# Kernel tuning notes

Measured on AMD Instinct MI355X. Metric: run time of the kernel, lower is better.

## Reference

```python
import jax, jax.numpy as jnp
import numpy as np

NEG_SLOPE = 0.2  # PyG GATConv LeakyReLU slope
BN_EPS = 1e-5
NUM_GRAPHS = 16


def gat_conv(x, src, dst, W, a_src, a_dst, bias, heads, out_c, concat):
    N = x.shape[0]
    h = (x @ W).reshape(N, heads, out_c)                      # [N,H,C]
    s_src = jnp.sum(h * a_src, axis=-1)                       # [N,H] per-node src score
    s_dst = jnp.sum(h * a_dst, axis=-1)                       # [N,H]
    e = jax.nn.leaky_relu(s_src[src] + s_dst[dst], NEG_SLOPE) # [E,H]
    # segment softmax over incoming edges of each dst node
    m = jax.ops.segment_max(e, dst, num_segments=N)           # [N,H]
    ex = jnp.exp(e - m[dst])
    denom = jax.ops.segment_sum(ex, dst, num_segments=N)      # [N,H]
    alpha = ex / (denom[dst] + 1e-16)                         # [E,H]
    msg = h[src] * alpha[:, :, None]                          # [E,H,C]
    out = jax.ops.segment_sum(msg, dst, num_segments=N)       # [N,H,C]
    out = out.reshape(N, heads * out_c) if concat else out.mean(axis=1)
    return out + bias


def batchnorm_eval(x, gamma, beta, rm, rv):
    return (x - rm) * jax.lax.rsqrt(rv + BN_EPS) * gamma + beta


def setup_inputs() -> dict:
    key = jax.random.key(0)
    ks = jax.random.split(key, 16)
    N, E, Fin, Hc, Hd, Emb = 20000, 640000, 128, 64, 4, 128
    x = jax.random.normal(ks[0], (N, Fin), dtype=jnp.float32)
    edge_index = jax.random.randint(ks[1], (2, E), 0, N, dtype=jnp.int64)
    batch = jnp.sort(jax.random.randint(ks[2], (N,), 0, NUM_GRAPHS, dtype=jnp.int64))
    sc1 = 1.0 / np.sqrt(Fin)
    sc2 = 1.0 / np.sqrt(Hc * Hd)
    return {
        "x": x, "edge_index": edge_index, "batch": batch,
        "W1": jax.random.normal(ks[3], (Fin, Hd * Hc), dtype=jnp.float32) * sc1,
        "a_src1": jax.random.normal(ks[4], (Hd, Hc), dtype=jnp.float32) * sc2,
        "a_dst1": jax.random.normal(ks[5], (Hd, Hc), dtype=jnp.float32) * sc2,
        "b1": jnp.zeros((Hd * Hc,), jnp.float32),
        "g1": jnp.ones((Hd * Hc,), jnp.float32),
        "be1": jnp.zeros((Hd * Hc,), jnp.float32),
        "rm1": jax.random.normal(ks[6], (Hd * Hc,), dtype=jnp.float32) * 0.1,
        "rv1": jnp.ones((Hd * Hc,), jnp.float32),
        "W2": jax.random.normal(ks[7], (Hd * Hc, Emb), dtype=jnp.float32) * sc2,
        "a_src2": jax.random.normal(ks[8], (1, Emb), dtype=jnp.float32) / np.sqrt(Emb),
        "a_dst2": jax.random.normal(ks[9], (1, Emb), dtype=jnp.float32) / np.sqrt(Emb),
        "b2": jnp.zeros((Emb,), jnp.float32),
        "g2": jnp.ones((Emb,), jnp.float32),
        "be2": jnp.zeros((Emb,), jnp.float32),
        "rm2": jax.random.normal(ks[10], (Emb,), dtype=jnp.float32) * 0.1,
        "rv2": jnp.ones((Emb,), jnp.float32),
    }


def reference(x, edge_index, batch, W1, a_src1, a_dst1, b1, g1, be1, rm1, rv1,
              W2, a_src2, a_dst2, b2, g2, be2, rm2, rv2):
    N = x.shape[0]
    loops = jnp.arange(N, dtype=edge_index.dtype)
    src = jnp.concatenate([edge_index[0], loops])  # PyG GATConv adds self-loops
    dst = jnp.concatenate([edge_index[1], loops])
    # layer 1: heads=4, concat
    h = gat_conv(x, src, dst, W1, a_src1, a_dst1, b1, heads=4, out_c=64, concat=True)
    h = batchnorm_eval(h, g1, be1, rm1, rv1)
    h = jax.nn.elu(h)  # dropout is identity in eval mode
    # layer 2: heads=1, no concat (mean over heads)
    h = gat_conv(h, src, dst, W2, a_src2, a_dst2, b2, heads=1, out_c=128, concat=False)
    h = batchnorm_eval(h, g2, be2, rm2, rv2)
    # global mean pool per graph
    sums = jax.ops.segment_sum(h, batch, num_segments=NUM_GRAPHS)
    cnts = jax.ops.segment_sum(jnp.ones((N,), h.dtype), batch, num_segments=NUM_GRAPHS)
    return sums / jnp.maximum(cnts, 1.0)[:, None]
```

## Files before the change

kernel.cpp:

```cpp
#include <hip/hip_runtime.h>
#include <hip/hip_bf16.h>
#include <math.h>

#define NEG_SLOPE 0.2f
#define BN_EPS 1e-5f
#define ELLW 128
#define SCLAMP 60.0f
#define LDP 68

typedef __attribute__((ext_vector_type(8))) short bf16x8;
typedef __attribute__((ext_vector_type(4))) float f32x4;

__device__ __forceinline__ void atomAddF(float* p, float v) { unsafeAtomicAdd(p, v); }
__device__ __forceinline__ float bf_lo(unsigned u) { return __uint_as_float(u << 16); }
__device__ __forceinline__ float bf_hi(unsigned u) { return __uint_as_float(u & 0xffff0000u); }
__device__ __forceinline__ float lk(float x) { return x > 0.f ? x : NEG_SLOPE * x; }
__device__ __forceinline__ float eexp(float x) { return __expf(fminf(x, SCLAMP)); }

__global__ __launch_bounds__(256) void prep_kernel(const float* __restrict__ x,
                                                   const float* __restrict__ W1,
                                                   const float* __restrict__ W2,
                                                   __hip_bfloat16* __restrict__ xbf,
                                                   __hip_bfloat16* __restrict__ WT1,
                                                   __hip_bfloat16* __restrict__ WT2,
                                                   int* __restrict__ zb, int zwords,
                                                   int n4) {
    int i = blockIdx.x * blockDim.x + threadIdx.x;
    if (i < n4) {
        float4 v = ((const float4*)x)[i];
        ushort4 st;
        st.x = __bfloat16_as_ushort(__float2bfloat16(v.x));
        st.y = __bfloat16_as_ushort(__float2bfloat16(v.y));
        st.z = __bfloat16_as_ushort(__float2bfloat16(v.z));
        st.w = __bfloat16_as_ushort(__float2bfloat16(v.w));
        *(ushort4*)(xbf + (size_t)i * 4) = st;
        return;
    }
    int j = i - n4;
    if (j < 128 * 256) {
        int k = j >> 8, n = j & 255;
        WT1[(size_t)n * 128 + k] = __float2bfloat16(W1[j]);
        return;
    }
    j -= 128 * 256;
    if (j < 256 * 128) {
        int k = j >> 7, n = j & 127;
        WT2[(size_t)n * 256 + k] = __float2bfloat16(W2[j]);
        return;
    }
    j -= 256 * 128;
    if (j < zwords) zb[j] = 0;
}

__global__ __launch_bounds__(256) void scatter_kernel(const int* __restrict__ src,
                                                      const int* __restrict__ dst,
                                                      int* __restrict__ cnt,
                                                      unsigned short* __restrict__ ell,
                                                      int N, int E, int Etot) {
    const int xcd = blockIdx.x & 7;
    const int slice = blockIdx.x >> 3;
    const int nslices = gridDim.x >> 3;
    const int d0 = (int)((long)xcd * N / 8);
    const int d1 = (int)((long)(xcd + 1) * N / 8);
    for (int e = slice * 256 + threadIdx.x; e < Etot; e += nslices * 256) {
        int d = (e < E) ? dst[e] : e - E;
        if (d < d0 || d >= d1) continue;
        int s = (e < E) ? src[e] : d;
        int pos = atomicAdd(cnt + d, 1);
        if (pos < ELLW) ell[(size_t)d * ELLW + pos] = (unsigned short)s;
    }
}

__global__ __launch_bounds__(256) void gemm_score_kernel(const __hip_bfloat16* __restrict__ A,
                                                         const __hip_bfloat16* __restrict__ BT,
                                                         __hip_bfloat16* __restrict__ C,
                                                         const float* __restrict__ asrc,
                                                         const float* __restrict__ adst,
                                                         float* __restrict__ ssrc,
                                                         float* __restrict__ sdst,
                                                         int M, int N, int K, int heads) {
    __shared__ __hip_bfloat16 As[64 * LDP];
    __shared__ __hip_bfloat16 Bs[64 * LDP];
    const int tid = threadIdx.x;
    const int w = tid >> 6;
    const int lane = tid & 63;
    const int q = lane >> 4;
    const int r16 = lane & 15;
    const int bm = blockIdx.y * 64;
    const int bn = blockIdx.x * 64;
    const int lrow = tid >> 3;
    const int lseg = tid & 7;
    f32x4 acc[4] = {};

    for (int k0 = 0; k0 < K; k0 += 64) {
#pragma unroll
        for (int half = 0; half < 2; ++half) {
            int row = lrow + half * 32;
            int ga = min(bm + row, M - 1);
            *(bf16x8*)(&As[row * LDP + lseg * 8]) =
                *(const bf16x8*)(A + (size_t)ga * K + k0 + lseg * 8);
            *(bf16x8*)(&Bs[row * LDP + lseg * 8]) =
                *(const bf16x8*)(BT + (size_t)(bn + row) * K + k0 + lseg * 8);
        }
        __syncthreads();
#pragma unroll
        for (int kk = 0; kk < 64; kk += 32) {
            bf16x8 a = *(const bf16x8*)(&As[(w * 16 + r16) * LDP + kk + q * 8]);
#pragma unroll
            for (int t = 0; t < 4; ++t) {
                bf16x8 b = *(const bf16x8*)(&Bs[(t * 16 + r16) * LDP + kk + q * 8]);
                acc[t] = __builtin_amdgcn_mfma_f32_16x16x32_bf16(a, b, acc[t], 0, 0, 0);
            }
        }
        __syncthreads();
    }
#pragma unroll
    for (int t = 0; t < 4; ++t)
#pragma unroll
        for (int r = 0; r < 4; ++r) {
            int row = bm + w * 16 + q * 4 + r;
            if (row < M)
                C[(size_t)row * N + bn + t * 16 + r16] = __float2bfloat16(acc[t][r]);
        }
    if (heads) {
        const int h = (heads == 4) ? blockIdx.x : 0;
        float asv[4], adv[4];
#pragma unroll
        for (int t = 0; t < 4; ++t) {
            int col = bn + t * 16 + r16;
            asv[t] = asrc[col]; adv[t] = adst[col];
        }
#pragma unroll
        for (int r = 0; r < 4; ++r) {
            int row = bm + w * 16 + q * 4 + r;
            float ss = 0.f, sd = 0.f;
#pragma unroll
            for (int t = 0; t < 4; ++t) { ss += acc[t][r] * asv[t]; sd += acc[t][r] * adv[t]; }
#pragma unroll
            for (int mask = 1; mask <= 8; mask <<= 1) {
                ss += __shfl_xor(ss, mask);
                sd += __shfl_xor(sd, mask);
            }
            if (r16 == 0 && row < M) {
                atomAddF(&ssrc[(size_t)row * heads + h], ss);
                atomAddF(&sdst[(size_t)row * heads + h], sd);
            }
        }
    }
}

__global__ __launch_bounds__(256) void fused1_kernel(const unsigned short* __restrict__ ell,
                                                     const int* __restrict__ cnt,
                                                     const float* __restrict__ ssrc,
                                                     const float* __restrict__ sdst,
                                                     const __hip_bfloat16* __restrict__ h1,
                                                     const float* __restrict__ b,
                                                     const float* __restrict__ g,
                                                     const float* __restrict__ be,
                                                     const float* __restrict__ rm,
                                                     const float* __restrict__ rv,
                                                     __hip_bfloat16* __restrict__ out1,
                                                     int N) {
    __shared__ float4 sex[4][ELLW];
    const int w = threadIdx.x >> 6;
    const int lane = threadIdx.x & 63;
    const int n = blockIdx.x * 4 + w;
    if (n >= N) return;
    const int degn = min(cnt[n], ELLW);
    const unsigned short* __restrict__ row = ell + (size_t)n * ELLW;
    const float4 sd4 = *(const float4*)(sdst + (size_t)n * 4);

    float4 d4 = {0.f, 0.f, 0.f, 0.f};
    for (int i = lane; i < degn; i += 64) {
        int s = row[i];
        float4 sc = *(const float4*)(ssrc + (size_t)s * 4);
        float4 e4;
        e4.x = eexp(lk(sc.x + sd4.x)); e4.y = eexp(lk(sc.y + sd4.y));
        e4.z = eexp(lk(sc.z + sd4.z)); e4.w = eexp(lk(sc.w + sd4.w));
        sex[w][i] = e4;
        d4.x += e4.x; d4.y += e4.y; d4.z += e4.z; d4.w += e4.w;
    }
#pragma unroll
    for (int o = 32; o; o >>= 1) {
        d4.x += __shfl_xor(d4.x, o); d4.y += __shfl_xor(d4.y, o);
        d4.z += __shfl_xor(d4.z, o); d4.w += __shfl_xor(d4.w, o);
    }

    const int h = lane >> 4, c16 = lane & 15;
    const int ch = h * 64 + c16 * 4;
    const float denh = h == 0 ? d4.x : h == 1 ? d4.y : h == 2 ? d4.z : d4.w;
    const float rden = 1.f / (denh + 1e-16f);
    const __hip_bfloat16* hbase = h1 + ch;
    const float* exw = (const float*)&sex[w][0];

    f32x4 acc = {0.f, 0.f, 0.f, 0.f};
    int i = 0;
    for (; i + 7 < degn; i += 8) {
        int s[8]; float a[8]; uint2 u[8];
#pragma unroll
        for (int k = 0; k < 8; ++k) { s[k] = row[i + k]; a[k] = exw[(i + k) * 4 + h]; }
#pragma unroll
        for (int k = 0; k < 8; ++k) u[k] = *(const uint2*)(hbase + (size_t)s[k] * 256);
#pragma unroll
        for (int k = 0; k < 8; ++k) {
            acc.x += a[k] * bf_lo(u[k].x); acc.y += a[k] * bf_hi(u[k].x);
            acc.z += a[k] * bf_lo(u[k].y); acc.w += a[k] * bf_hi(u[k].y);
        }
    }
    for (; i < degn; ++i) {
        int s0 = row[i];
        float a0 = exw[i * 4 + h];
        uint2 u0 = *(const uint2*)(hbase + (size_t)s0 * 256);
        acc.x += a0 * bf_lo(u0.x); acc.y += a0 * bf_hi(u0.x);
        acc.z += a0 * bf_lo(u0.y); acc.w += a0 * bf_hi(u0.y);
    }
    float4 bb = *(const float4*)(b + ch), gg = *(const float4*)(g + ch);
    float4 ee = *(const float4*)(be + ch), mm = *(const float4*)(rm + ch);
    float4 vv = *(const float4*)(rv + ch);
    float o0 = (acc.x * rden + bb.x - mm.x) * rsqrtf(vv.x + BN_EPS) * gg.x + ee.x;
    float o1 = (acc.y * rden + bb.y - mm.y) * rsqrtf(vv.y + BN_EPS) * gg.y + ee.y;
    float o2 = (acc.z * rden + bb.z - mm.z) * rsqrtf(vv.z + BN_EPS) * gg.z + ee.z;
    float o3 = (acc.w * rden + bb.w - mm.w) * rsqrtf(vv.w + BN_EPS) * gg.w + ee.w;
    o0 = o0 > 0.f ? o0 : expm1f(o0);
    o1 = o1 > 0.f ? o1 : expm1f(o1);
    o2 = o2 > 0.f ? o2 : expm1f(o2);
    o3 = o3 > 0.f ? o3 : expm1f(o3);
    ushort4 st;
    st.x = __bfloat16_as_ushort(__float2bfloat16(o0));
    st.y = __bfloat16_as_ushort(__float2bfloat16(o1));
    st.z = __bfloat16_as_ushort(__float2bfloat16(o2));
    st.w = __bfloat16_as_ushort(__float2bfloat16(o3));
    *(ushort4*)(out1 + (size_t)n * 256 + ch) = st;
}

__global__ __launch_bounds__(256) void fused2_kernel(const unsigned short* __restrict__ ell,
                                                     const int* __restrict__ cnt,
                                                     const float* __restrict__ ssrc,
                                                     const float* __restrict__ sdst,
                                                     const __hip_bfloat16* __restrict__ h2,
                                                     const float* __restrict__ b,
                                                     const float* __restrict__ g,
                                                     const float* __restrict__ be,
                                                     const float* __restrict__ rm,
                                                     const float* __restrict__ rv,
                                                     __hip_bfloat16* __restrict__ out2,
                                                     int N) {
    __shared__ float sex[4][ELLW];
    const int w = threadIdx.x >> 6;
    const int lane = threadIdx.x & 63;
    const int n = blockIdx.x * 4 + w;
    if (n >= N) return;
    const int degn = min(cnt[n], ELLW);
    const unsigned short* __restrict__ row = ell + (size_t)n * ELLW;
    const float sd = sdst[n];

    float den = 0.f;
    for (int i = lane; i < degn; i += 64) {
        int s = row[i];
        float e = eexp(lk(ssrc[s] + sd));
        sex[w][i] = e;
        den += e;
    }
#pragma unroll
    for (int o = 32; o; o >>= 1) den += __shfl_xor(den, o);
    const float rden = 1.f / (den + 1e-16f);

    const int ch = lane * 2;
    const __hip_bfloat16* hbase = h2 + ch;
    float ax = 0.f, ay = 0.f;
    int i = 0;
    for (; i + 7 < degn; i += 8) {
        int s[8]; float a[8]; unsigned u[8];
#pragma unroll
        for (int k = 0; k < 8; ++k) { s[k] = row[i + k]; a[k] = sex[w][i + k]; }
#pragma unroll
        for (int k = 0; k < 8; ++k) u[k] = *(const unsigned*)(hbase + (size_t)s[k] * 128);
#pragma unroll
        for (int k = 0; k < 8; ++k) { ax += a[k] * bf_lo(u[k]); ay += a[k] * bf_hi(u[k]); }
    }
    for (; i < degn; ++i) {
        int s0 = row[i];
        float a0 = sex[w][i];
        unsigned u0 = *(const unsigned*)(hbase + (size_t)s0 * 128);
        ax += a0 * bf_lo(u0); ay += a0 * bf_hi(u0);
    }
    float2 bb = *(const float2*)(b + ch), gg = *(const float2*)(g + ch);
    float2 ee = *(const float2*)(be + ch), mm = *(const float2*)(rm + ch);
    float2 vv = *(const float2*)(rv + ch);
    float ox = (ax * rden + bb.x - mm.x) * rsqrtf(vv.x + BN_EPS) * gg.x + ee.x;
    float oy = (ay * rden + bb.y - mm.y) * rsqrtf(vv.y + BN_EPS) * gg.y + ee.y;
    ushort2 st;
    st.x = __bfloat16_as_ushort(__float2bfloat16(ox));
    st.y = __bfloat16_as_ushort(__float2bfloat16(oy));
    *(ushort2*)(out2 + (size_t)n * 128 + ch) = st;
}

__global__ __launch_bounds__(128) void pool_kernel(const __hip_bfloat16* __restrict__ out2,
                                                   const int* __restrict__ batch,
                                                   float* __restrict__ pool,
                                                   int N, int npb) {
    const int j = threadIdx.x;
    int n0 = blockIdx.x * npb;
    int n1 = min(n0 + npb, N);
    if (n0 >= n1) return;
    int curg = batch[n0];
    float acc = 0.f;
    for (int n = n0; n < n1; ++n) {
        int gr = batch[n];
        if (gr != curg) {
            atomAddF(pool + (size_t)curg * 128 + j, acc);
            acc = 0.f; curg = gr;
        }
        acc += __bfloat162float(out2[(size_t)n * 128 + j]);
    }
    atomAddF(pool + (size_t)curg * 128 + j, acc);
}

__device__ __forceinline__ int lowerBound(const int* __restrict__ a, int n, int v) {
    int lo = 0, hi = n;
    while (lo < hi) {
        int mid = (lo + hi) >> 1;
        if (a[mid] < v) lo = mid + 1; else hi = mid;
    }
    return lo;
}

__global__ __launch_bounds__(256) void final_kernel(const float* __restrict__ pool,
                                                    const int* __restrict__ batch,
                                                    float* __restrict__ out, int N) {
    int i = blockIdx.x * blockDim.x + threadIdx.x;
    int g = i >> 7;
    int c = lowerBound(batch, N, g + 1) - lowerBound(batch, N, g);
    out[i] = pool[i] / fmaxf((float)c, 1.f);
}

extern "C" void kernel_launch(void* const* d_in, const int* in_sizes, int n_in,
                              void* d_out, int out_size, void* d_ws, size_t ws_size,
                              hipStream_t stream) {
    const float* x    = (const float*)d_in[0];
    const int* ei     = (const int*)d_in[1];
    const int* batch  = (const int*)d_in[2];
    const float* W1   = (const float*)d_in[3];
    const float* as1  = (const float*)d_in[4];
    const float* ad1  = (const float*)d_in[5];
    const float* b1   = (const float*)d_in[6];
    const float* g1   = (const float*)d_in[7];
    const float* be1  = (const float*)d_in[8];
    const float* rm1  = (const float*)d_in[9];
    const float* rv1  = (const float*)d_in[10];
    const float* W2   = (const float*)d_in[11];
    const float* as2  = (const float*)d_in[12];
    const float* ad2  = (const float*)d_in[13];
    const float* b2   = (const float*)d_in[14];
    const float* g2   = (const float*)d_in[15];
    const float* be2  = (const float*)d_in[16];
    const float* rm2  = (const float*)d_in[17];
    const float* rv2  = (const float*)d_in[18];
    float* out = (float*)d_out;

    const int N = in_sizes[0] / 128;
    const int E = in_sizes[1] / 2;
    const int Etot = E + N;
    const int* src = ei;
    const int* dst = ei + E;

    char* p = (char*)d_ws;
    auto alloc = [&](size_t bytes) { char* r = p; p += (bytes + 255) & ~(size_t)255; return r; };
    __hip_bfloat16* h1   = (__hip_bfloat16*)alloc((size_t)N * 256 * 2);
    __hip_bfloat16* out1 = (__hip_bfloat16*)alloc((size_t)N * 256 * 2);
    __hip_bfloat16* out2 = (__hip_bfloat16*)alloc((size_t)N * 128 * 2);
    __hip_bfloat16* xbf  = (__hip_bfloat16*)alloc((size_t)N * 128 * 2);
    __hip_bfloat16* WT1  = (__hip_bfloat16*)alloc(256 * 128 * 2);
    __hip_bfloat16* WT2  = (__hip_bfloat16*)alloc(128 * 256 * 2);
    const int zwords     = N * 10 + 2048 + N;
    char* zbase          = alloc((size_t)zwords * 4);
    float* ssrc1         = (float*)zbase;
    float* sdst1         = ssrc1 + (size_t)N * 4;
    float* ssrc2         = sdst1 + (size_t)N * 4;
    float* sdst2         = ssrc2 + N;
    float* pool          = sdst2 + N;
    int*   cnt           = (int*)(pool + 2048);
    unsigned short* ell  = (unsigned short*)alloc((size_t)N * ELLW * 2);
    __hip_bfloat16* h2   = h1;

    const int n4 = N * 128 / 4;
    const int ptot = n4 + 2 * 128 * 256 + zwords;
    prep_kernel<<<(ptot + 255) / 256, 256, 0, stream>>>(x, W1, W2, xbf, WT1, WT2,
                                                        (int*)zbase, zwords, n4);
    scatter_kernel<<<2048, 256, 0, stream>>>(src, dst, cnt, ell, N, E, Etot);

    gemm_score_kernel<<<dim3(256 / 64, (N + 63) / 64), 256, 0, stream>>>(
        xbf, WT1, h1, as1, ad1, ssrc1, sdst1, N, 256, 128, 4);
    fused1_kernel<<<(N + 3) / 4, 256, 0, stream>>>(ell, cnt, ssrc1, sdst1, h1,
                                                   b1, g1, be1, rm1, rv1, out1, N);
    gemm_score_kernel<<<dim3(128 / 64, (N + 63) / 64), 256, 0, stream>>>(
        out1, WT2, h2, as2, ad2, ssrc2, sdst2, N, 128, 256, 1);
    fused2_kernel<<<(N + 3) / 4, 256, 0, stream>>>(ell, cnt, ssrc2, sdst2, h2,
                                                   b2, g2, be2, rm2, rv2, out2, N);

    pool_kernel<<<(N + 19) / 20, 128, 0, stream>>>(out2, batch, pool, N, 20);
    final_kernel<<<8, 256, 0, stream>>>(pool, batch, out, N);
}
```

Baseline: 239.9 us.

## Widen neighbor gathers to 16B per lane and fuse pooling into layer-2 aggregation

```diff
diff --git a/kernel.cpp b/kernel.cpp
--- a/kernel.cpp
+++ b/kernel.cpp
@@ -16,6 +16,10 @@
 __device__ __forceinline__ float bf_hi(unsigned u) { return __uint_as_float(u & 0xffff0000u); }
 __device__ __forceinline__ float lk(float x) { return x > 0.f ? x : NEG_SLOPE * x; }
 __device__ __forceinline__ float eexp(float x) { return __expf(fminf(x, SCLAMP)); }
+__device__ __forceinline__ unsigned packbf(float lo, float hi) {
+    return (unsigned)__bfloat16_as_ushort(__float2bfloat16(lo)) |
+           ((unsigned)__bfloat16_as_ushort(__float2bfloat16(hi)) << 16);
+}
 
 __global__ __launch_bounds__(256) void prep_kernel(const float* __restrict__ x,
                                                    const float* __restrict__ W1,
@@ -161,7 +165,8 @@
                                                      const float* __restrict__ rv,
                                                      __hip_bfloat16* __restrict__ out1,
                                                      int N) {
-    __shared__ float4 sex[4][ELLW];
+    __shared__ float sex[4][ELLW * 4];
+    __shared__ unsigned soff[4][ELLW];
     const int w = threadIdx.x >> 6;
     const int lane = threadIdx.x & 63;
     const int n = blockIdx.x * 4 + w;
@@ -177,8 +182,14 @@
         float4 e4;
         e4.x = eexp(lk(sc.x + sd4.x)); e4.y = eexp(lk(sc.y + sd4.y));
         e4.z = eexp(lk(sc.z + sd4.z)); e4.w = eexp(lk(sc.w + sd4.w));
-        sex[w][i] = e4;
+        *(float4*)(&sex[w][i * 4]) = e4;
+        soff[w][i] = (unsigned)s << 9;
         d4.x += e4.x; d4.y += e4.y; d4.z += e4.z; d4.w += e4.w;
+    }
+    if (lane == 0 && (degn & 1)) {
+        float4 z = {0.f, 0.f, 0.f, 0.f};
+        *(float4*)(&sex[w][degn * 4]) = z;
+        soff[w][degn] = 0;
     }
 #pragma unroll
     for (int o = 32; o; o >>= 1) {
@@ -186,51 +197,74 @@
         d4.z += __shfl_xor(d4.z, o); d4.w += __shfl_xor(d4.w, o);
     }
 
-    const int h = lane >> 4, c16 = lane & 15;
-    const int ch = h * 64 + c16 * 4;
+    const int half = lane >> 5;
+    const int l32 = lane & 31;
+    const int ch = l32 * 8;
+    const int h = l32 >> 3;
+    const unsigned choff = (unsigned)(l32 * 16);
     const float denh = h == 0 ? d4.x : h == 1 ? d4.y : h == 2 ? d4.z : d4.w;
     const float rden = 1.f / (denh + 1e-16f);
-    const __hip_bfloat16* hbase = h1 + ch;
-    const float* exw = (const float*)&sex[w][0];
-
-    f32x4 acc = {0.f, 0.f, 0.f, 0.f};
+    const unsigned char* __restrict__ hb = (const unsigned char*)h1;
+    const int degp = (degn + 1) & ~1;
+
+    f32x4 a0 = {0.f, 0.f, 0.f, 0.f}, a1 = {0.f, 0.f, 0.f, 0.f};
     int i = 0;
-    for (; i + 7 < degn; i += 8) {
-        int s[8]; float a[8]; uint2 u[8];
-#pragma unroll
-        for (int k = 0; k < 8; ++k) { s[k] = row[i + k]; a[k] = exw[(i + k) * 4 + h]; }
-#pragma unroll
-        for (int k = 0; k < 8; ++k) u[k] = *(const uint2*)(hbase + (size_t)s[k] * 256);
-#pragma unroll
-        for (int k = 0; k < 8; ++k) {
-            acc.x += a[k] * bf_lo(u[k].x); acc.y += a[k] * bf_hi(u[k].x);
-            acc.z += a[k] * bf_lo(u[k].y); acc.w += a[k] * bf_hi(u[k].y);
-        }
-    }
-    for (; i < degn; ++i) {
-        int s0 = row[i];
-        float a0 = exw[i * 4 + h];
-        uint2 u0 = *(const uint2*)(hbase + (size_t)s0 * 256);
-        acc.x += a0 * bf_lo(u0.x); acc.y += a0 * bf_hi(u0.x);
-        acc.z += a0 * bf_lo(u0.y); acc.w += a0 * bf_hi(u0.y);
-    }
-    float4 bb = *(const float4*)(b + ch), gg = *(const float4*)(g + ch);
-    float4 ee = *(const float4*)(be + ch), mm = *(const float4*)(rm + ch);
-    float4 vv = *(const float4*)(rv + ch);
-    float o0 = (acc.x * rden + bb.x - mm.x) * rsqrtf(vv.x + BN_EPS) * gg.x + ee.x;
-    float o1 = (acc.y * rden + bb.y - mm.y) * rsqrtf(vv.y + BN_EPS) * gg.y + ee.y;
-    float o2 = (acc.z * rden + bb.z - mm.z) * rsqrtf(vv.z + BN_EPS) * gg.z + ee.z;
-    float o3 = (acc.w * rden + bb.w - mm.w) * rsqrtf(vv.w + BN_EPS) * gg.w + ee.w;
-    o0 = o0 > 0.f ? o0 : expm1f(o0);
-    o1 = o1 > 0.f ? o1 : expm1f(o1);
-    o2 = o2 > 0.f ? o2 : expm1f(o2);
-    o3 = o3 > 0.f ? o3 : expm1f(o3);
-    ushort4 st;
-    st.x = __bfloat16_as_ushort(__float2bfloat16(o0));
-    st.y = __bfloat16_as_ushort(__float2bfloat16(o1));
-    st.z = __bfloat16_as_ushort(__float2bfloat16(o2));
-    st.w = __bfloat16_as_ushort(__float2bfloat16(o3));
-    *(ushort4*)(out1 + (size_t)n * 256 + ch) = st;
+    for (; i + 8 <= degp; i += 8) {
+        unsigned off[4]; float av[4]; uint4 u[4];
+#pragma unroll
+        for (int k = 0; k < 4; ++k) {
+            int e = i + 2 * k + half;
+            off[k] = soff[w][e] + choff;
+            av[k] = sex[w][e * 4 + h];
+        }
+#pragma unroll
+        for (int k = 0; k < 4; ++k) u[k] = *(const uint4*)(hb + off[k]);
+#pragma unroll
+        for (int k = 0; k < 4; ++k) {
+            a0.x += av[k] * bf_lo(u[k].x); a0.y += av[k] * bf_hi(u[k].x);
+            a0.z += av[k] * bf_lo(u[k].y); a0.w += av[k] * bf_hi(u[k].y);
+            a1.x += av[k] * bf_lo(u[k].z); a1.y += av[k] * bf_hi(u[k].z);
+            a1.z += av[k] * bf_lo(u[k].w); a1.w += av[k] * bf_hi(u[k].w);
+        }
+    }
+    for (; i < degp; i += 2) {
+        int e = i + half;
+        unsigned off = soff[w][e] + choff;
+        float av = sex[w][e * 4 + h];
+        uint4 u = *(const uint4*)(hb + off);
+        a0.x += av * bf_lo(u.x); a0.y += av * bf_hi(u.x);
+        a0.z += av * bf_lo(u.y); a0.w += av * bf_hi(u.y);
+        a1.x += av * bf_lo(u.z); a1.y += av * bf_hi(u.z);
+        a1.z += av * bf_lo(u.w); a1.w += av * bf_hi(u.w);
+    }
+    a0.x += __shfl_xor(a0.x, 32); a0.y += __shfl_xor(a0.y, 32);
+    a0.z += __shfl_xor(a0.z, 32); a0.w += __shfl_xor(a0.w, 32);
+    a1.x += __shfl_xor(a1.x, 32); a1.y += __shfl_xor(a1.y, 32);
+    a1.z += __shfl_xor(a1.z, 32); a1.w += __shfl_xor(a1.w, 32);
+
+    float4 bb0 = *(const float4*)(b + ch),  bb1 = *(const float4*)(b + ch + 4);
+    float4 gg0 = *(const float4*)(g + ch),  gg1 = *(const float4*)(g + ch + 4);
+    float4 ee0 = *(const float4*)(be + ch), ee1 = *(const float4*)(be + ch + 4);
+    float4 mm0 = *(const float4*)(rm + ch), mm1 = *(const float4*)(rm + ch + 4);
+    float4 vv0 = *(const float4*)(rv + ch), vv1 = *(const float4*)(rv + ch + 4);
+    float o0 = (a0.x * rden + bb0.x - mm0.x) * rsqrtf(vv0.x + BN_EPS) * gg0.x + ee0.x;
+    float o1 = (a0.y * rden + bb0.y - mm0.y) * rsqrtf(vv0.y + BN_EPS) * gg0.y + ee0.y;
+    float o2 = (a0.z * rden + bb0.z - mm0.z) * rsqrtf(vv0.z + BN_EPS) * gg0.z + ee0.z;
+    float o3 = (a0.w * rden + bb0.w - mm0.w) * rsqrtf(vv0.w + BN_EPS) * gg0.w + ee0.w;
+    float o4 = (a1.x * rden + bb1.x - mm1.x) * rsqrtf(vv1.x + BN_EPS) * gg1.x + ee1.x;
+    float o5 = (a1.y * rden + bb1.y - mm1.y) * rsqrtf(vv1.y + BN_EPS) * gg1.y + ee1.y;
+    float o6 = (a1.z * rden + bb1.z - mm1.z) * rsqrtf(vv1.z + BN_EPS) * gg1.z + ee1.z;
+    float o7 = (a1.w * rden + bb1.w - mm1.w) * rsqrtf(vv1.w + BN_EPS) * gg1.w + ee1.w;
+    o0 = o0 > 0.f ? o0 : expm1f(o0); o1 = o1 > 0.f ? o1 : expm1f(o1);
+    o2 = o2 > 0.f ? o2 : expm1f(o2); o3 = o3 > 0.f ? o3 : expm1f(o3);
+    o4 = o4 > 0.f ? o4 : expm1f(o4); o5 = o5 > 0.f ? o5 : expm1f(o5);
+    o6 = o6 > 0.f ? o6 : expm1f(o6); o7 = o7 > 0.f ? o7 : expm1f(o7);
+    if (half == 0) {
+        uint4 st;
+        st.x = packbf(o0, o1); st.y = packbf(o2, o3);
+        st.z = packbf(o4, o5); st.w = packbf(o6, o7);
+        *(uint4*)(out1 + (size_t)n * 256 + ch) = st;
+    }
 }
 
 __global__ __launch_bounds__(256) void fused2_kernel(const unsigned short* __restrict__ ell,
@@ -243,9 +277,11 @@
                                                      const float* __restrict__ be,
                                                      const float* __restrict__ rm,
                                                      const float* __restrict__ rv,
-                                                     __hip_bfloat16* __restrict__ out2,
+                                                     const int* __restrict__ batch,
+                                                     float* __restrict__ pool,
                                                      int N) {
     __shared__ float sex[4][ELLW];
+    __shared__ unsigned soff[4][ELLW];
     const int w = threadIdx.x >> 6;
     const int lane = threadIdx.x & 63;
     const int n = blockIdx.x * 4 + w;
@@ -259,61 +295,62 @@
         int s = row[i];
         float e = eexp(lk(ssrc[s] + sd));
         sex[w][i] = e;
+        soff[w][i] = (unsigned)s << 8;
         den += e;
     }
+    if (lane == 0 && (degn & 1)) { sex[w][degn] = 0.f; soff[w][degn] = 0; }
 #pragma unroll
     for (int o = 32; o; o >>= 1) den += __shfl_xor(den, o);
     const float rden = 1.f / (den + 1e-16f);
 
-    const int ch = lane * 2;
-    const __hip_bfloat16* hbase = h2 + ch;
-    float ax = 0.f, ay = 0.f;
+    const int half = lane >> 5;
+    const int l32 = lane & 31;
+    const int ch = l32 * 4;
+    const unsigned choff = (unsigned)(l32 * 8);
+    const unsigned char* __restrict__ hb = (const unsigned char*)h2;
+    const int degp = (degn + 1) & ~1;
+
+    f32x4 acc = {0.f, 0.f, 0.f, 0.f};
     int i = 0;
-    for (; i + 7 < degn; i += 8) {
-        int s[8]; float a[8]; unsigned u[8];
-#pragma unroll
-        for (int k = 0; k < 8; ++k) { s[k] = row[i + k]; a[k] = sex[w][i + k]; }
-#pragma unroll
-        for (int k = 0; k < 8; ++k) u[k] = *(const unsigned*)(hbase + (size_t)s[k] * 128);
-#pragma unroll
-        for (int k = 0; k < 8; ++k) { ax += a[k] * bf_lo(u[k]); ay += a[k] * bf_hi(u[k]); }
-    }
-    for (; i < degn; ++i) {
-        int s0 = row[i];
-        float a0 = sex[w][i];
-        unsigned u0 = *(const unsigned*)(hbase + (size_t)s0 * 128);
-        ax += a0 * bf_lo(u0); ay += a0 * bf_hi(u0);
-    }
-    float2 bb = *(const float2*)(b + ch), gg = *(const float2*)(g + ch);
-    float2 ee = *(const float2*)(be + ch), mm = *(const float2*)(rm + ch);
-    float2 vv = *(const float2*)(rv + ch);
-    float ox = (ax * rden + bb.x - mm.x) * rsqrtf(vv.x + BN_EPS) * gg.x + ee.x;
-    float oy = (ay * rden + bb.y - mm.y) * rsqrtf(vv.y + BN_EPS) * gg.y + ee.y;
-    ushort2 st;
-    st.x = __bfloat16_as_ushort(__float2bfloat16(ox));
-    st.y = __bfloat16_as_ushort(__float2bfloat16(oy));
-    *(ushort2*)(out2 + (size_t)n * 128 + ch) = st;
-}
-
-__global__ __launch_bounds__(128) void pool_kernel(const __hip_bfloat16* __restrict__ out2,
-                                                   const int* __restrict__ batch,
-                                                   float* __restrict__ pool,
-                                                   int N, int npb) {
-    const int j = threadIdx.x;
-    int n0 = blockIdx.x * npb;
-    int n1 = min(n0 + npb, N);
-    if (n0 >= n1) return;
-    int curg = batch[n0];
-    float acc = 0.f;
-    for (int n = n0; n < n1; ++n) {
-        int gr = batch[n];
-        if (gr != curg) {
-            atomAddF(pool + (size_t)curg * 128 + j, acc);
-            acc = 0.f; curg = gr;
-        }
-        acc += __bfloat162float(out2[(size_t)n * 128 + j]);
-    }
-    atomAddF(pool + (size_t)curg * 128 + j, acc);
+    for (; i + 8 <= degp; i += 8) {
+        unsigned off[4]; float av[4]; uint2 u[4];
+#pragma unroll
+        for (int k = 0; k < 4; ++k) {
+            int e = i + 2 * k + half;
+            off[k] = soff[w][e] + choff;
+            av[k] = sex[w][e];
+        }
+#pragma unroll
+        for (int k = 0; k < 4; ++k) u[k] = *(const uint2*)(hb + off[k]);
+#pragma unroll
+        for (int k = 0; k < 4; ++k) {
+            acc.x += av[k] * bf_lo(u[k].x); acc.y += av[k] * bf_hi(u[k].x);
+            acc.z += av[k] * bf_lo(u[k].y); acc.w += av[k] * bf_hi(u[k].y);
+        }
+    }
+    for (; i < degp; i += 2) {
+        int e = i + half;
+        unsigned off = soff[w][e] + choff;
+        float av = sex[w][e];
+        uint2 u = *(const uint2*)(hb + off);
+        acc.x += av * bf_lo(u.x); acc.y += av * bf_hi(u.x);
+        acc.z += av * bf_lo(u.y); acc.w += av * bf_hi(u.y);
+    }
+    acc.x += __shfl_xor(acc.x, 32); acc.y += __shfl_xor(acc.y, 32);
+    acc.z += __shfl_xor(acc.z, 32); acc.w += __shfl_xor(acc.w, 32);
+
+    if (half == 0) {
+        float4 bb = *(const float4*)(b + ch), gg = *(const float4*)(g + ch);
+        float4 ee = *(const float4*)(be + ch), mm = *(const float4*)(rm + ch);
+        float4 vv = *(const float4*)(rv + ch);
+        float o0 = (acc.x * rden + bb.x - mm.x) * rsqrtf(vv.x + BN_EPS) * gg.x + ee.x;
+        float o1 = (acc.y * rden + bb.y - mm.y) * rsqrtf(vv.y + BN_EPS) * gg.y + ee.y;
+        float o2 = (acc.z * rden + bb.z - mm.z) * rsqrtf(vv.z + BN_EPS) * gg.z + ee.z;
+        float o3 = (acc.w * rden + bb.w - mm.w) * rsqrtf(vv.w + BN_EPS) * gg.w + ee.w;
+        float* pp = pool + (size_t)batch[n] * 128 + ch;
+        atomAddF(pp + 0, o0); atomAddF(pp + 1, o1);
+        atomAddF(pp + 2, o2); atomAddF(pp + 3, o3);
+    }
 }
 
 __device__ __forceinline__ int lowerBound(const int* __restrict__ a, int n, int v) {
@@ -368,7 +405,6 @@
     auto alloc = [&](size_t bytes) { char* r = p; p += (bytes + 255) & ~(size_t)255; return r; };
     __hip_bfloat16* h1   = (__hip_bfloat16*)alloc((size_t)N * 256 * 2);
     __hip_bfloat16* out1 = (__hip_bfloat16*)alloc((size_t)N * 256 * 2);
-    __hip_bfloat16* out2 = (__hip_bfloat16*)alloc((size_t)N * 128 * 2);
     __hip_bfloat16* xbf  = (__hip_bfloat16*)alloc((size_t)N * 128 * 2);
     __hip_bfloat16* WT1  = (__hip_bfloat16*)alloc(256 * 128 * 2);
     __hip_bfloat16* WT2  = (__hip_bfloat16*)alloc(128 * 256 * 2);
@@ -396,8 +432,7 @@
     gemm_score_kernel<<<dim3(128 / 64, (N + 63) / 64), 256, 0, stream>>>(
         out1, WT2, h2, as2, ad2, ssrc2, sdst2, N, 128, 256, 1);
     fused2_kernel<<<(N + 3) / 4, 256, 0, stream>>>(ell, cnt, ssrc2, sdst2, h2,
-                                                   b2, g2, be2, rm2, rv2, out2, N);
-
-    pool_kernel<<<(N + 19) / 20, 128, 0, stream>>>(out2, batch, pool, N, 20);
+                                                   b2, g2, be2, rm2, rv2, batch, pool, N);
+
     final_kernel<<<8, 256, 0, stream>>>(pool, batch, out, N);
 }
```

After: 462.9 us. +93.0%, slower.

## Store GEMM output head-sliced, split aggregation per head, merge scatter with GEMM

Applied to the files above, without the earlier changes.

```diff
diff --git a/kernel.cpp b/kernel.cpp
--- a/kernel.cpp
+++ b/kernel.cpp
@@ -16,6 +16,10 @@
 __device__ __forceinline__ float bf_hi(unsigned u) { return __uint_as_float(u & 0xffff0000u); }
 __device__ __forceinline__ float lk(float x) { return x > 0.f ? x : NEG_SLOPE * x; }
 __device__ __forceinline__ float eexp(float x) { return __expf(fminf(x, SCLAMP)); }
+__device__ __forceinline__ unsigned packbf(float lo, float hi) {
+    return (unsigned)__bfloat16_as_ushort(__float2bfloat16(lo)) |
+           ((unsigned)__bfloat16_as_ushort(__float2bfloat16(hi)) << 16);
+}
 
 __global__ __launch_bounds__(256) void prep_kernel(const float* __restrict__ x,
                                                    const float* __restrict__ W1,
@@ -52,14 +56,108 @@
     if (j < zwords) zb[j] = 0;
 }
 
-__global__ __launch_bounds__(256) void scatter_kernel(const int* __restrict__ src,
-                                                      const int* __restrict__ dst,
-                                                      int* __restrict__ cnt,
-                                                      unsigned short* __restrict__ ell,
-                                                      int N, int E, int Etot) {
-    const int xcd = blockIdx.x & 7;
-    const int slice = blockIdx.x >> 3;
-    const int nslices = gridDim.x >> 3;
+__device__ __forceinline__ void gemm_body(const __hip_bfloat16* __restrict__ A,
+                                          const __hip_bfloat16* __restrict__ BT,
+                                          __hip_bfloat16* __restrict__ C,
+                                          const float* __restrict__ asrc,
+                                          const float* __restrict__ adst,
+                                          float* __restrict__ ssrc,
+                                          float* __restrict__ sdst,
+                                          int M, int N, int K, int heads,
+                                          int bx, int by) {
+    __shared__ __hip_bfloat16 As[64 * LDP];
+    __shared__ __hip_bfloat16 Bs[64 * LDP];
+    const int tid = threadIdx.x;
+    const int w = tid >> 6;
+    const int lane = tid & 63;
+    const int q = lane >> 4;
+    const int r16 = lane & 15;
+    const int bm = by * 64;
+    const int bn = bx * 64;
+    const int lrow = tid >> 3;
+    const int lseg = tid & 7;
+    f32x4 acc[4] = {};
+
+    for (int k0 = 0; k0 < K; k0 += 64) {
+#pragma unroll
+        for (int half = 0; half < 2; ++half) {
+            int row = lrow + half * 32;
+            int ga = min(bm + row, M - 1);
+            *(bf16x8*)(&As[row * LDP + lseg * 8]) =
+                *(const bf16x8*)(A + (size_t)ga * K + k0 + lseg * 8);
+            *(bf16x8*)(&Bs[row * LDP + lseg * 8]) =
+                *(const bf16x8*)(BT + (size_t)(bn + row) * K + k0 + lseg * 8);
+        }
+        __syncthreads();
+#pragma unroll
+        for (int kk = 0; kk < 64; kk += 32) {
+            bf16x8 a = *(const bf16x8*)(&As[(w * 16 + r16) * LDP + kk + q * 8]);
+#pragma unroll
+            for (int t = 0; t < 4; ++t) {
+                bf16x8 b = *(const bf16x8*)(&Bs[(t * 16 + r16) * LDP + kk + q * 8]);
+                acc[t] = __builtin_amdgcn_mfma_f32_16x16x32_bf16(a, b, acc[t], 0, 0, 0);
+            }
+        }
+        __syncthreads();
+    }
+    const size_t sbase = (size_t)(bn >> 6) * M * 64;
+#pragma unroll
+    for (int t = 0; t < 4; ++t)
+#pragma unroll
+        for (int r = 0; r < 4; ++r) {
+            int row = bm + w * 16 + q * 4 + r;
+            if (row < M)
+                C[sbase + (size_t)row * 64 + t * 16 + r16] = __float2bfloat16(acc[t][r]);
+        }
+    if (heads) {
+        const int h = (heads == 4) ? bx : 0;
+        float asv[4], adv[4];
+#pragma unroll
+        for (int t = 0; t < 4; ++t) {
+            int col = bn + t * 16 + r16;
+            asv[t] = asrc[col]; adv[t] = adst[col];
+        }
+#pragma unroll
+        for (int r = 0; r < 4; ++r) {
+            int row = bm + w * 16 + q * 4 + r;
+            float ss = 0.f, sd = 0.f;
+#pragma unroll
+            for (int t = 0; t < 4; ++t) { ss += acc[t][r] * asv[t]; sd += acc[t][r] * adv[t]; }
+#pragma unroll
+            for (int mask = 1; mask <= 8; mask <<= 1) {
+                ss += __shfl_xor(ss, mask);
+                sd += __shfl_xor(sd, mask);
+            }
+            if (r16 == 0 && row < M) {
+                atomAddF(&ssrc[(size_t)row * heads + h], ss);
+                atomAddF(&sdst[(size_t)row * heads + h], sd);
+            }
+        }
+    }
+}
+
+__global__ __launch_bounds__(256) void sg1_kernel(const __hip_bfloat16* __restrict__ A,
+                                                  const __hip_bfloat16* __restrict__ BT,
+                                                  __hip_bfloat16* __restrict__ C,
+                                                  const float* __restrict__ asrc,
+                                                  const float* __restrict__ adst,
+                                                  float* __restrict__ ssrc,
+                                                  float* __restrict__ sdst,
+                                                  int M, int nbg,
+                                                  const int* __restrict__ src,
+                                                  const int* __restrict__ dst,
+                                                  int* __restrict__ cnt,
+                                                  unsigned short* __restrict__ ell,
+                                                  int N, int E, int Etot) {
+    const int gb = blockIdx.x;
+    if (gb < nbg) {
+        gemm_body(A, BT, C, asrc, adst, ssrc, sdst, M, 256, 128, 4, gb & 3, gb >> 2);
+        return;
+    }
+    const int xcd = gb & 7;
+    const int sb = gb - nbg;
+    const int slice = sb >> 3;
+    const int nslices = (gridDim.x - nbg) >> 3;
     const int d0 = (int)((long)xcd * N / 8);
     const int d1 = (int)((long)(xcd + 1) * N / 8);
     for (int e = slice * 256 + threadIdx.x; e < Etot; e += nslices * 256) {
@@ -79,74 +177,7 @@
                                                          float* __restrict__ ssrc,
                                                          float* __restrict__ sdst,
                                                          int M, int N, int K, int heads) {
-    __shared__ __hip_bfloat16 As[64 * LDP];
-    __shared__ __hip_bfloat16 Bs[64 * LDP];
-    const int tid = threadIdx.x;
-    const int w = tid >> 6;
-    const int lane = tid & 63;
-    const int q = lane >> 4;
-    const int r16 = lane & 15;
-    const int bm = blockIdx.y * 64;
-    const int bn = blockIdx.x * 64;
-    const int lrow = tid >> 3;
-    const int lseg = tid & 7;
-    f32x4 acc[4] = {};
-
-    for (int k0 = 0; k0 < K; k0 += 64) {
-#pragma unroll
-        for (int half = 0; half < 2; ++half) {
-            int row = lrow + half * 32;
-            int ga = min(bm + row, M - 1);
-            *(bf16x8*)(&As[row * LDP + lseg * 8]) =
-                *(const bf16x8*)(A + (size_t)ga * K + k0 + lseg * 8);
-            *(bf16x8*)(&Bs[row * LDP + lseg * 8]) =
-                *(const bf16x8*)(BT + (size_t)(bn + row) * K + k0 + lseg * 8);
-        }
-        __syncthreads();
-#pragma unroll
-        for (int kk = 0; kk < 64; kk += 32) {
-            bf16x8 a = *(const bf16x8*)(&As[(w * 16 + r16) * LDP + kk + q * 8]);
-#pragma unroll
-            for (int t = 0; t < 4; ++t) {
-                bf16x8 b = *(const bf16x8*)(&Bs[(t * 16 + r16) * LDP + kk + q * 8]);
-                acc[t] = __builtin_amdgcn_mfma_f32_16x16x32_bf16(a, b, acc[t], 0, 0, 0);
-            }
-        }
-        __syncthreads();
-    }
-#pragma unroll
-    for (int t = 0; t < 4; ++t)
-#pragma unroll
-        for (int r = 0; r < 4; ++r) {
-            int row = bm + w * 16 + q * 4 + r;
-            if (row < M)
-                C[(size_t)row * N + bn + t * 16 + r16] = __float2bfloat16(acc[t][r]);
-        }
-    if (heads) {
-        const int h = (heads == 4) ? blockIdx.x : 0;
-        float asv[4], adv[4];
-#pragma unroll
-        for (int t = 0; t < 4; ++t) {
-            int col = bn + t * 16 + r16;
-            asv[t] = asrc[col]; adv[t] = adst[col];
-        }
-#pragma unroll
-        for (int r = 0; r < 4; ++r) {
-            int row = bm + w * 16 + q * 4 + r;
-            float ss = 0.f, sd = 0.f;
-#pragma unroll
-            for (int t = 0; t < 4; ++t) { ss += acc[t][r] * asv[t]; sd += acc[t][r] * adv[t]; }
-#pragma unroll
-            for (int mask = 1; mask <= 8; mask <<= 1) {
-                ss += __shfl_xor(ss, mask);
-                sd += __shfl_xor(sd, mask);
-            }
-            if (r16 == 0 && row < M) {
-                atomAddF(&ssrc[(size_t)row * heads + h], ss);
-                atomAddF(&sdst[(size_t)row * heads + h], sd);
-            }
-        }
-    }
+    gemm_body(A, BT, C, asrc, adst, ssrc, sdst, M, N, K, heads, blockIdx.x, blockIdx.y);
 }
 
 __global__ __launch_bounds__(256) void fused1_kernel(const unsigned short* __restrict__ ell,
@@ -161,76 +192,82 @@
                                                      const float* __restrict__ rv,
                                                      __hip_bfloat16* __restrict__ out1,
                                                      int N) {
-    __shared__ float4 sex[4][ELLW];
+    __shared__ float sex[4][ELLW];
+    __shared__ unsigned soff[4][ELLW];
     const int w = threadIdx.x >> 6;
     const int lane = threadIdx.x & 63;
     const int n = blockIdx.x * 4 + w;
+    const int h = blockIdx.y;
     if (n >= N) return;
     const int degn = min(cnt[n], ELLW);
     const unsigned short* __restrict__ row = ell + (size_t)n * ELLW;
-    const float4 sd4 = *(const float4*)(sdst + (size_t)n * 4);
-
-    float4 d4 = {0.f, 0.f, 0.f, 0.f};
+    const float sd = sdst[n * 4 + h];
+
+    float den = 0.f;
     for (int i = lane; i < degn; i += 64) {
         int s = row[i];
-        float4 sc = *(const float4*)(ssrc + (size_t)s * 4);
-        float4 e4;
-        e4.x = eexp(lk(sc.x + sd4.x)); e4.y = eexp(lk(sc.y + sd4.y));
-        e4.z = eexp(lk(sc.z + sd4.z)); e4.w = eexp(lk(sc.w + sd4.w));
-        sex[w][i] = e4;
-        d4.x += e4.x; d4.y += e4.y; d4.z += e4.z; d4.w += e4.w;
-    }
-#pragma unroll
-    for (int o = 32; o; o >>= 1) {
-        d4.x += __shfl_xor(d4.x, o); d4.y += __shfl_xor(d4.y, o);
-        d4.z += __shfl_xor(d4.z, o); d4.w += __shfl_xor(d4.w, o);
-    }
-
-    const int h = lane >> 4, c16 = lane & 15;
-    const int ch = h * 64 + c16 * 4;
-    const float denh = h == 0 ? d4.x : h == 1 ? d4.y : h == 2 ? d4.z : d4.w;
-    const float rden = 1.f / (denh + 1e-16f);
-    const __hip_bfloat16* hbase = h1 + ch;
-    const float* exw = (const float*)&sex[w][0];
-
-    f32x4 acc = {0.f, 0.f, 0.f, 0.f};
-    int i = 0;
-    for (; i + 7 < degn; i += 8) {
-        int s[8]; float a[8]; uint2 u[8];
-#pragma unroll
-        for (int k = 0; k < 8; ++k) { s[k] = row[i + k]; a[k] = exw[(i + k) * 4 + h]; }
-#pragma unroll
-        for (int k = 0; k < 8; ++k) u[k] = *(const uint2*)(hbase + (size_t)s[k] * 256);
-#pragma unroll
-        for (int k = 0; k < 8; ++k) {
-            acc.x += a[k] * bf_lo(u[k].x); acc.y += a[k] * bf_hi(u[k].x);
-            acc.z += a[k] * bf_lo(u[k].y); acc.w += a[k] * bf_hi(u[k].y);
-        }
-    }
-    for (; i < degn; ++i) {
-        int s0 = row[i];
-        float a0 = exw[i * 4 + h];
-        uint2 u0 = *(const uint2*)(hbase + (size_t)s0 * 256);
-        acc.x += a0 * bf_lo(u0.x); acc.y += a0 * bf_hi(u0.x);
-        acc.z += a0 * bf_lo(u0.y); acc.w += a0 * bf_hi(u0.y);
-    }
-    float4 bb = *(const float4*)(b + ch), gg = *(const float4*)(g + ch);
-    float4 ee = *(const float4*)(be + ch), mm = *(const float4*)(rm + ch);
-    float4 vv = *(const float4*)(rv + ch);
-    float o0 = (acc.x * rden + bb.x - mm.x) * rsqrtf(vv.x + BN_EPS) * gg.x + ee.x;
-    float o1 = (acc.y * rden + bb.y - mm.y) * rsqrtf(vv.y + BN_EPS) * gg.y + ee.y;
-    float o2 = (acc.z * rden + bb.z - mm.z) * rsqrtf(vv.z + BN_EPS) * gg.z + ee.z;
-    float o3 = (acc.w * rden + bb.w - mm.w) * rsqrtf(vv.w + BN_EPS) * gg.w + ee.w;
-    o0 = o0 > 0.f ? o0 : expm1f(o0);
-    o1 = o1 > 0.f ? o1 : expm1f(o1);
-    o2 = o2 > 0.f ? o2 : expm1f(o2);
-    o3 = o3 > 0.f ? o3 : expm1f(o3);
-    ushort4 st;
-    st.x = __bfloat16_as_ushort(__float2bfloat16(o0));
-    st.y = __bfloat16_as_ushort(__float2bfloat16(o1));
-    st.z = __bfloat16_as_ushort(__float2bfloat16(o2));
-    st.w = __bfloat16_as_ushort(__float2bfloat16(o3));
-    *(ushort4*)(out1 + (size_t)n * 256 + ch) = st;
+        float e = eexp(lk(ssrc[s * 4 + h] + sd));
+        sex[w][i] = e;
+        soff[w][i] = (unsigned)s << 7;
+        den += e;
+    }
+    const int degp = (degn + 15) & ~15;
+    for (int i = degn + lane; i < degp; i += 64) { sex[w][i] = 0.f; soff[w][i] = 0; }
+#pragma unroll
+    for (int o = 32; o; o >>= 1) den += __shfl_xor(den, o);
+    const float rden = 1.f / (den + 1e-16f);
+
+    const int eg = lane >> 3;
+    const int cc = lane & 7;
+    const unsigned choff = (unsigned)cc * 16;
+    const unsigned char* __restrict__ hb =
+        (const unsigned char*)(h1 + (size_t)h * N * 64);
+
+    float acc[8] = {};
+    for (int i = 0; i < degp; i += 16) {
+        int e0 = i + eg, e1 = i + 8 + eg;
+        float av0 = sex[w][e0], av1 = sex[w][e1];
+        unsigned o0 = soff[w][e0] + choff, o1 = soff[w][e1] + choff;
+        uint4 u0 = *(const uint4*)(hb + o0);
+        uint4 u1 = *(const uint4*)(hb + o1);
+        acc[0] += av0 * bf_lo(u0.x); acc[1] += av0 * bf_hi(u0.x);
+        acc[2] += av0 * bf_lo(u0.y); acc[3] += av0 * bf_hi(u0.y);
+        acc[4] += av0 * bf_lo(u0.z); acc[5] += av0 * bf_hi(u0.z);
+        acc[6] += av0 * bf_lo(u0.w); acc[7] += av0 * bf_hi(u0.w);
+        acc[0] += av1 * bf_lo(u1.x); acc[1] += av1 * bf_hi(u1.x);
+        acc[2] += av1 * bf_lo(u1.y); acc[3] += av1 * bf_hi(u1.y);
+        acc[4] += av1 * bf_lo(u1.z); acc[5] += av1 * bf_hi(u1.z);
+        acc[6] += av1 * bf_lo(u1.w); acc[7] += av1 * bf_hi(u1.w);
+    }
+#pragma unroll
+    for (int m = 8; m <= 32; m <<= 1)
+#pragma unroll
+        for (int j = 0; j < 8; ++j) acc[j] += __shfl_xor(acc[j], m);
+
+    if (eg == 0) {
+        const int ch = h * 64 + cc * 8;
+        float4 bb0 = *(const float4*)(b + ch),  bb1 = *(const float4*)(b + ch + 4);
+        float4 gg0 = *(const float4*)(g + ch),  gg1 = *(const float4*)(g + ch + 4);
+        float4 ee0 = *(const float4*)(be + ch), ee1 = *(const float4*)(be + ch + 4);
+        float4 mm0 = *(const float4*)(rm + ch), mm1 = *(const float4*)(rm + ch + 4);
+        float4 vv0 = *(const float4*)(rv + ch), vv1 = *(const float4*)(rv + ch + 4);
+        float o0 = (acc[0] * rden + bb0.x - mm0.x) * rsqrtf(vv0.x + BN_EPS) * gg0.x + ee0.x;
+        float o1 = (acc[1] * rden + bb0.y - mm0.y) * rsqrtf(vv0.y + BN_EPS) * gg0.y + ee0.y;
+        float o2 = (acc[2] * rden + bb0.z - mm0.z) * rsqrtf(vv0.z + BN_EPS) * gg0.z + ee0.z;
+        float o3 = (acc[3] * rden + bb0.w - mm0.w) * rsqrtf(vv0.w + BN_EPS) * gg0.w + ee0.w;
+        float o4 = (acc[4] * rden + bb1.x - mm1.x) * rsqrtf(vv1.x + BN_EPS) * gg1.x + ee1.x;
+        float o5 = (acc[5] * rden + bb1.y - mm1.y) * rsqrtf(vv1.y + BN_EPS) * gg1.y + ee1.y;
+        float o6 = (acc[6] * rden + bb1.z - mm1.z) * rsqrtf(vv1.z + BN_EPS) * gg1.z + ee1.z;
+        float o7 = (acc[7] * rden + bb1.w - mm1.w) * rsqrtf(vv1.w + BN_EPS) * gg1.w + ee1.w;
+        o0 = o0 > 0.f ? o0 : expm1f(o0); o1 = o1 > 0.f ? o1 : expm1f(o1);
+        o2 = o2 > 0.f ? o2 : expm1f(o2); o3 = o3 > 0.f ? o3 : expm1f(o3);
+        o4 = o4 > 0.f ? o4 : expm1f(o4); o5 = o5 > 0.f ? o5 : expm1f(o5);
+        o6 = o6 > 0.f ? o6 : expm1f(o6); o7 = o7 > 0.f ? o7 : expm1f(o7);
+        uint4 st;
+        st.x = packbf(o0, o1); st.y = packbf(o2, o3);
+        st.z = packbf(o4, o5); st.w = packbf(o6, o7);
+        *(uint4*)(out1 + (size_t)n * 256 + ch) = st;
+    }
 }
 
 __global__ __launch_bounds__(256) void fused2_kernel(const unsigned short* __restrict__ ell,
@@ -246,9 +283,11 @@
                                                      __hip_bfloat16* __restrict__ out2,
                                                      int N) {
     __shared__ float sex[4][ELLW];
+    __shared__ unsigned soff[4][ELLW];
     const int w = threadIdx.x >> 6;
     const int lane = threadIdx.x & 63;
     const int n = blockIdx.x * 4 + w;
+    const int hf = blockIdx.y;
     if (n >= N) return;
     const int degn = min(cnt[n], ELLW);
     const unsigned short* __restrict__ row = ell + (size_t)n * ELLW;
@@ -259,40 +298,62 @@
         int s = row[i];
         float e = eexp(lk(ssrc[s] + sd));
         sex[w][i] = e;
+        soff[w][i] = (unsigned)s << 7;
         den += e;
     }
+    const int degp = (degn + 15) & ~15;
+    for (int i = degn + lane; i < degp; i += 64) { sex[w][i] = 0.f; soff[w][i] = 0; }
 #pragma unroll
     for (int o = 32; o; o >>= 1) den += __shfl_xor(den, o);
     const float rden = 1.f / (den + 1e-16f);
 
-    const int ch = lane * 2;
-    const __hip_bfloat16* hbase = h2 + ch;
-    float ax = 0.f, ay = 0.f;
-    int i = 0;
-    for (; i + 7 < degn; i += 8) {
-        int s[8]; float a[8]; unsigned u[8];
-#pragma unroll
-        for (int k = 0; k < 8; ++k) { s[k] = row[i + k]; a[k] = sex[w][i + k]; }
-#pragma unroll
-        for (int k = 0; k < 8; ++k) u[k] = *(const unsigned*)(hbase + (size_t)s[k] * 128);
-#pragma unroll
-        for (int k = 0; k < 8; ++k) { ax += a[k] * bf_lo(u[k]); ay += a[k] * bf_hi(u[k]); }
-    }
-    for (; i < degn; ++i) {
-        int s0 = row[i];
-        float a0 = sex[w][i];
-        unsigned u0 = *(const unsigned*)(hbase + (size_t)s0 * 128);
-        ax += a0 * bf_lo(u0); ay += a0 * bf_hi(u0);
-    }
-    float2 bb = *(const float2*)(b + ch), gg = *(const float2*)(g + ch);
-    float2 ee = *(const float2*)(be + ch), mm = *(const float2*)(rm + ch);
-    float2 vv = *(const float2*)(rv + ch);
-    float ox = (ax * rden + bb.x - mm.x) * rsqrtf(vv.x + BN_EPS) * gg.x + ee.x;
-    float oy = (ay * rden + bb.y - mm.y) * rsqrtf(vv.y + BN_EPS) * gg.y + ee.y;
-    ushort2 st;
-    st.x = __bfloat16_as_ushort(__float2bfloat16(ox));
-    st.y = __bfloat16_as_ushort(__float2bfloat16(oy));
-    *(ushort2*)(out2 + (size_t)n * 128 + ch) = st;
+    const int eg = lane >> 3;
+    const int cc = lane & 7;
+    const unsigned choff = (unsigned)cc * 16;
+    const unsigned char* __restrict__ hb =
+        (const unsigned char*)(h2 + (size_t)hf * N * 64);
+
+    float acc[8] = {};
+    for (int i = 0; i < degp; i += 16) {
+        int e0 = i + eg, e1 = i + 8 + eg;
+        float av0 = sex[w][e0], av1 = sex[w][e1];
+        unsigned o0 = soff[w][e0] + choff, o1 = soff[w][e1] + choff;
+        uint4 u0 = *(const uint4*)(hb + o0);
+        uint4 u1 = *(const uint4*)(hb + o1);
+        acc[0] += av0 * bf_lo(u0.x); acc[1] += av0 * bf_hi(u0.x);
+        acc[2] += av0 * bf_lo(u0.y); acc[3] += av0 * bf_hi(u0.y);
+        acc[4] += av0 * bf_lo(u0.z); acc[5] += av0 * bf_hi(u0.z);
+        acc[6] += av0 * bf_lo(u0.w); acc[7] += av0 * bf_hi(u0.w);
+        acc[0] += av1 * bf_lo(u1.x); acc[1] += av1 * bf_hi(u1.x);
+        acc[2] += av1 * bf_lo(u1.y); acc[3] += av1 * bf_hi(u1.y);
+        acc[4] += av1 * bf_lo(u1.z); acc[5] += av1 * bf_hi(u1.z);
+        acc[6] += av1 * bf_lo(u1.w); acc[7] += av1 * bf_hi(u1.w);
+    }
+#pragma unroll
+    for (int m = 8; m <= 32; m <<= 1)
+#pragma unroll
+        for (int j = 0; j < 8; ++j) acc[j] += __shfl_xor(acc[j], m);
+
+    if (eg == 0) {
+        const int ch = hf * 64 + cc * 8;
+        float4 bb0 = *(const float4*)(b + ch),  bb1 = *(const float4*)(b + ch + 4);
+        float4 gg0 = *(const float4*)(g + ch),  gg1 = *(const float4*)(g + ch + 4);
+        float4 ee0 = *(const float4*)(be + ch), ee1 = *(const float4*)(be + ch + 4);
+        float4 mm0 = *(const float4*)(rm + ch), mm1 = *(const float4*)(rm + ch + 4);
+        float4 vv0 = *(const float4*)(rv + ch), vv1 = *(const float4*)(rv + ch + 4);
+        float o0 = (acc[0] * rden + bb0.x - mm0.x) * rsqrtf(vv0.x + BN_EPS) * gg0.x + ee0.x;
+        float o1 = (acc[1] * rden + bb0.y - mm0.y) * rsqrtf(vv0.y + BN_EPS) * gg0.y + ee0.y;
+        float o2 = (acc[2] * rden + bb0.z - mm0.z) * rsqrtf(vv0.z + BN_EPS) * gg0.z + ee0.z;
+        float o3 = (acc[3] * rden + bb0.w - mm0.w) * rsqrtf(vv0.w + BN_EPS) * gg0.w + ee0.w;
+        float o4 = (acc[4] * rden + bb1.x - mm1.x) * rsqrtf(vv1.x + BN_EPS) * gg1.x + ee1.x;
+        float o5 = (acc[5] * rden + bb1.y - mm1.y) * rsqrtf(vv1.y + BN_EPS) * gg1.y + ee1.y;
+        float o6 = (acc[6] * rden + bb1.z - mm1.z) * rsqrtf(vv1.z + BN_EPS) * gg1.z + ee1.z;
+        float o7 = (acc[7] * rden + bb1.w - mm1.w) * rsqrtf(vv1.w + BN_EPS) * gg1.w + ee1.w;
+        uint4 st;
+        st.x = packbf(o0, o1); st.y = packbf(o2, o3);
+        st.z = packbf(o4, o5); st.w = packbf(o6, o7);
+        *(uint4*)(out2 + (size_t)n * 128 + ch) = st;
+    }
 }
 
 __global__ __launch_bounds__(128) void pool_kernel(const __hip_bfloat16* __restrict__ out2,
@@ -387,16 +448,17 @@
     const int ptot = n4 + 2 * 128 * 256 + zwords;
     prep_kernel<<<(ptot + 255) / 256, 256, 0, stream>>>(x, W1, W2, xbf, WT1, WT2,
                                                         (int*)zbase, zwords, n4);
-    scatter_kernel<<<2048, 256, 0, stream>>>(src, dst, cnt, ell, N, E, Etot);
-
-    gemm_score_kernel<<<dim3(256 / 64, (N + 63) / 64), 256, 0, stream>>>(
-        xbf, WT1, h1, as1, ad1, ssrc1, sdst1, N, 256, 128, 4);
-    fused1_kernel<<<(N + 3) / 4, 256, 0, stream>>>(ell, cnt, ssrc1, sdst1, h1,
-                                                   b1, g1, be1, rm1, rv1, out1, N);
+
+    const int nbg1 = 4 * ((N + 63) / 64);
+    sg1_kernel<<<nbg1 + 2048, 256, 0, stream>>>(xbf, WT1, h1, as1, ad1, ssrc1, sdst1,
+                                                N, nbg1, src, dst, cnt, ell, N, E, Etot);
+
+    fused1_kernel<<<dim3((N + 3) / 4, 4), 256, 0, stream>>>(ell, cnt, ssrc1, sdst1, h1,
+                                                            b1, g1, be1, rm1, rv1, out1, N);
     gemm_score_kernel<<<dim3(128 / 64, (N + 63) / 64), 256, 0, stream>>>(
         out1, WT2, h2, as2, ad2, ssrc2, sdst2, N, 128, 256, 1);
-    fused2_kernel<<<(N + 3) / 4, 256, 0, stream>>>(ell, cnt, ssrc2, sdst2, h2,
-                                                   b2, g2, be2, rm2, rv2, out2, N);
+    fused2_kernel<<<dim3((N + 3) / 4, 2), 256, 0, stream>>>(ell, cnt, ssrc2, sdst2, h2,
+                                                            b2, g2, be2, rm2, rv2, out2, N);
 
     pool_kernel<<<(N + 19) / 20, 128, 0, stream>>>(out2, batch, pool, N, 20);
     final_kernel<<<8, 256, 0, stream>>>(pool, batch, out, N);
```

Result: slower. 256.5 us (+6.9%).
